# Kernel optimization log

Hardware: AMD Instinct MI355X
Metric: run time of the kernel (lower is better)

The kernel has to match this reference:

```python
import jax, jax.numpy as jnp
import numpy as np
from jax import lax

SHIFTS = (1, 2, 4, 8)

def _neighbors(x, d):
    # x: [B,C,H,W] -> [B,8,C,H,W], 8 reflection-padded directional shifts
    H, W = x.shape[2], x.shape[3]
    def p(t, l, b, r):
        return jnp.pad(x, ((0, 0), (0, 0), (t, b), (l, r)), mode='reflect')
    x0 = p(d, d, 0, 0)[:, :, :H, :W]
    x1 = p(d, 0, 0, 0)[:, :, :H, :]
    x2 = p(d, 0, 0, d)[:, :, :H, d:]
    x3 = p(0, d, 0, 0)[:, :, :, :W]
    x4 = p(0, 0, 0, d)[:, :, :, d:]
    x5 = p(0, d, d, 0)[:, :, d:, :W]
    x6 = p(0, 0, d, 0)[:, :, d:, :]
    x7 = p(0, 0, d, d)[:, :, d:, d:]
    return jnp.stack([x0, x1, x2, x3, x4, x5, x6, x7], axis=1)

def _l2norm(x):
    # F.normalize(dim=-1): x / max(||x||, 1e-12)
    n = jnp.sqrt(jnp.sum(x * x, axis=-1, keepdims=True))
    return x / jnp.maximum(n, 1e-12)

def _forward(cen, q_w, k_w, v_w, sur_w1, sur_b1, sur_w2, sur_b2, sum_weights, out_w, bn_gamma, bn_beta):
    B, C, H, W = cen.shape
    nh = len(SHIFTS)
    keys, qrys, vals = [], [], []
    for i, d in enumerate(SHIFTS):
        nb = _neighbors(cen, d)  # [B,8,C,H,W]
        w2 = jax.nn.softmax(sum_weights[i])  # [2]
        h1 = lax.conv_general_dilated(cen, sur_w1[i], (1, 1), ((d, d), (d, d)),
                                      rhs_dilation=(d, d),
                                      dimension_numbers=('NCHW', 'OIHW', 'NCHW'))
        h1 = jax.nn.relu(h1 + sur_b1[i][None, :, None, None])
        sw = jax.nn.softmax(jnp.einsum('bchw,oc->bohw', h1, sur_w2[i]) + sur_b2[i][None, :, None, None], axis=1) * w2[0]  # [B,8,H,W]
        sum_x = jnp.einsum('bkchw,bkhw->bchw', nb, sw) + cen * w2[1]
        cen_x = nb.mean(axis=1) * w2[0] + cen * w2[1]
        sur = (nb - sum_x[:, None]).reshape(B, 8 * C, H, W)  # cat of x_k - sum_x
        keys.append(jnp.einsum('bchw,oc->bohw', sur, k_w[i]))    # [B,8*hid,H,W]
        vals.append(jnp.einsum('bchw,oc->bohw', sur, v_w[i]))
        qrys.append(jnp.einsum('bchw,oc->bohw', cen_x, q_w[i]))  # [B,hid,H,W]
    HW = H * W
    # torch.stack(dim=2).view(b, nh, -1, HW): row-major reinterpretation
    K = jnp.stack(keys, axis=2).reshape(B, nh, -1, HW)
    Q = jnp.stack(qrys, axis=2).reshape(B, nh, -1, HW)
    V = jnp.stack(vals, axis=2).reshape(B, nh, -1, HW)
    K = _l2norm(K)
    Q = _l2norm(Q)
    score = jnp.einsum('bnqs,bnks->bnqk', Q, K) / np.float32(np.sqrt(HW))
    # InstanceNorm2d(nh), affine=False: normalize over last two dims per (b, head)
    mu = score.mean(axis=(-2, -1), keepdims=True)
    var = score.var(axis=(-2, -1), keepdims=True)
    score = (score - mu) * lax.rsqrt(var + 1e-5)
    attn = jax.nn.softmax(score, axis=-1)
    out = jnp.einsum('bnqk,bnks->bnqs', attn, V).reshape(B, -1, H, W)  # [B,tra,H,W]
    y = jnp.einsum('bchw,oc->bohw', out, out_w)
    # BatchNorm2d in training mode (batch statistics)
    m = y.mean(axis=(0, 2, 3), keepdims=True)
    v = y.var(axis=(0, 2, 3), keepdims=True)
    y = (y - m) * lax.rsqrt(v + 1e-5) * bn_gamma[None, :, None, None] + bn_beta[None, :, None, None]
    return jax.nn.relu(y)

def setup_inputs() -> dict:
    key = jax.random.key(0)
    ks = jax.random.split(key, 12)
    B, C, H, W = 2, 32, 128, 128
    nh, hid, tra, oc = 4, 64, 256, 256
    r = lambda k, s, sc: jax.random.normal(k, s, dtype=jnp.float32) * sc
    return {
        'cen': r(ks[0], (B, C, H, W), 1.0),
        'q_w': r(ks[1], (nh, hid, C), 0.05),
        'k_w': r(ks[2], (nh, 8 * hid, 8 * C), 0.05),
        'v_w': r(ks[3], (nh, 8 * hid, 8 * C), 0.05),
        'sur_w1': r(ks[4], (nh, C, C, 3, 3), 0.05),
        'sur_b1': r(ks[5], (nh, C), 0.02),
        'sur_w2': r(ks[6], (nh, 8, C), 0.05),
        'sur_b2': r(ks[7], (nh, 8), 0.02),
        'sum_weights': r(ks[8], (nh, 2), 0.1),
        'out_w': r(ks[9], (oc, tra), 0.05),
        'bn_gamma': jnp.ones((oc,), jnp.float32) + r(ks[10], (oc,), 0.05),
        'bn_beta': r(ks[11], (oc,), 0.05),
    }

def reference(cen, q_w, k_w, v_w, sur_w1, sur_b1, sur_w2, sur_b2, sum_weights, out_w, bn_gamma, bn_beta):
    return _forward(cen, q_w, k_w, v_w, sur_w1, sur_b1, sur_w2, sur_b2, sum_weights, out_w, bn_gamma, bn_beta)
```

## Files before the change

### kernel.cpp

```cpp
#include <hip/hip_runtime.h>


#define HW 16384
typedef unsigned short u16;
typedef unsigned int u32;
typedef __attribute__((ext_vector_type(8))) short short8;
typedef __attribute__((ext_vector_type(4))) float f32x4;

#define S_CEN 0
#define S_QW 1048576
#define S_KW 1056768
#define S_VW 1581056
#define S_W1 2105344
#define S_B1 2142208
#define S_W2 2142336
#define S_B2 2143360
#define S_SW 2143392
#define S_OW 2143400
#define S_GAMMA 2208936
#define S_BETA 2209192
#define S_TOTAL 2209456

#define G_D1 0
#define G_D2 16384
#define G_S 147456
#define G_SZ 409600

#define GP_SLOT 344064

__device__ __forceinline__ float b2f(u16 u) { return __uint_as_float(((u32)u) << 16); }
__device__ __forceinline__ u16 f2b(float f) {
  u32 u = __float_as_uint(f);
  return (u16)((u + 0x7FFFu + ((u >> 16) & 1u)) >> 16);
}
__device__ __forceinline__ float wave_sum(float v) {
  #pragma unroll
  for (int off = 32; off > 0; off >>= 1) v += __shfl_xor(v, off, 64);
  return v;
}
__device__ __forceinline__ float wave_max(float v) {
  #pragma unroll
  for (int off = 32; off > 0; off >>= 1) v = fmaxf(v, __shfl_xor(v, off, 64));
  return v;
}
__device__ __forceinline__ void unpack8(uint4 v, float* f) {
  f[0] = __uint_as_float(v.x << 16); f[1] = __uint_as_float(v.x & 0xFFFF0000u);
  f[2] = __uint_as_float(v.y << 16); f[3] = __uint_as_float(v.y & 0xFFFF0000u);
  f[4] = __uint_as_float(v.z << 16); f[5] = __uint_as_float(v.z & 0xFFFF0000u);
  f[6] = __uint_as_float(v.w << 16); f[7] = __uint_as_float(v.w & 0xFFFF0000u);
}
__device__ __forceinline__ void gload16(const u16* g, u16* l) {
  __builtin_amdgcn_global_load_lds(
      (const __attribute__((address_space(1))) void*)g,
      (__attribute__((address_space(3))) void*)l, 16, 0, 0);
}

__device__ __forceinline__ void tile_decode(int tile, int& r0, int& c0,
                                            size_t& goff, int& gstride) {
  if (tile == 0) { r0 = 0; c0 = 0; goff = G_D1; gstride = 128; }
  else if (tile < 9) { r0 = 0; c0 = 128 * tile; goff = G_D2 + (size_t)(tile - 1) * 128; gstride = 1024; }
  else if (tile < 17) {
    int t2 = tile - 9; int j = t2 >> 1, p = t2 & 1;
    r0 = 128 + 256 * j + 128 * p; c0 = r0;
    goff = G_S + (size_t)j * 65536 + (size_t)p * (128 * 256 + 128); gstride = 256;
  } else {
    int j = tile - 17;
    r0 = 128 + 256 * j; c0 = r0 + 128;
    goff = G_S + (size_t)j * 65536 + 128; gstride = 256;
  }
}

__global__ void probe(const u32* __restrict__ g, int* __restrict__ flag) {
  if (threadIdx.x == 0) {
    int ok = 1;
    #pragma unroll
    for (int i = 0; i < 4; i++) {
      u32 w = g[i];
      u32 lo = w & 0xFFFFu, hi = w >> 16;
      ok &= (lo >= 0x3E00u && lo <= 0x4100u) ? 1 : 0;
      ok &= (hi >= 0x3E00u && hi <= 0x4100u) ? 1 : 0;
    }
    *flag = ok ? 0 : 1;
  }
}

__global__ __launch_bounds__(256) void convert_all(
    const void* p0, const void* p1, const void* p2, const void* p3,
    const void* p4, const void* p5, const void* p6, const void* p7,
    const void* p8, const void* p9, const void* p10, const void* p11,
    u16* __restrict__ S, const int* __restrict__ flag) {
  const void* src; int n; int off;
  switch (blockIdx.z) {
    case 0:  src = p0;  n = 1048576; off = S_CEN; break;
    case 1:  src = p1;  n = 8192;    off = S_QW; break;
    case 2:  src = p2;  n = 524288;  off = S_KW; break;
    case 3:  src = p3;  n = 524288;  off = S_VW; break;
    case 4:  src = p4;  n = 36864;   off = S_W1; break;
    case 5:  src = p5;  n = 128;     off = S_B1; break;
    case 6:  src = p6;  n = 1024;    off = S_W2; break;
    case 7:  src = p7;  n = 32;      off = S_B2; break;
    case 8:  src = p8;  n = 8;       off = S_SW; break;
    case 9:  src = p9;  n = 65536;   off = S_OW; break;
    case 10: src = p10; n = 256;     off = S_GAMMA; break;
    default: src = p11; n = 256;     off = S_BETA; break;
  }
  int idx = (blockIdx.x * 256 + threadIdx.x) * 4;
  if (idx >= n) return;
  u16* dst = S + off + idx;
  if (*flag) {
    float4 v = ((const float4*)src)[idx >> 2];
    dst[0] = f2b(v.x); dst[1] = f2b(v.y); dst[2] = f2b(v.z); dst[3] = f2b(v.w);
  } else {
    *(ushort4*)dst = ((const ushort4*)src)[idx >> 2];
  }
}

__global__ __launch_bounds__(256) void transp(
    const u16* __restrict__ cen, u16* __restrict__ cenT) {
  __shared__ u16 tile[32][258];
  const int t = threadIdx.x;
  const int s0 = blockIdx.x * 256;
  const u16* cb = cen + (size_t)blockIdx.y * 32 * HW;
  for (int e = t; e < 2048; e += 256) {
    int ci = e >> 6, sx = (e & 63) * 4;
    *(u32*)&tile[ci][sx] = *(const u32*)&cb[(size_t)ci * HW + s0 + sx];
    *(u32*)&tile[ci][sx + 2] = *(const u32*)&cb[(size_t)ci * HW + s0 + sx + 2];
  }
  __syncthreads();
  u16* ob = cenT + (size_t)blockIdx.y * HW * 32;
  for (int e = t; e < 1024; e += 256) {
    int px = e >> 2, cg = (e & 3) * 8;
    u16 tmp[8];
    #pragma unroll
    for (int k = 0; k < 8; k++) tmp[k] = tile[cg + k][px];
    *(uint4*)&ob[(size_t)(s0 + px) * 32 + cg] = *(uint4*)tmp;
  }
}

__global__ __launch_bounds__(256) void sur_w(
    const u16* __restrict__ cenT, const u16* __restrict__ w1g,
    const u16* __restrict__ b1g, const u16* __restrict__ w2g,
    const u16* __restrict__ zbuf, float* __restrict__ lgbuf) {
  const int z = blockIdx.y;
  const int b = z >> 2, si = z & 3, d = 1 << si;
  const int hh = blockIdx.x;
  __shared__ __align__(16) char smem[27776];
  u16* Bs = (u16*)smem;
  u16* w1s = (u16*)(smem + 8192);
  float* h1s = (float*)smem;
  __shared__ float w2s[8][32];
  __shared__ float b1s[32];
  const int t = threadIdx.x;
  for (int e = t; e < 9216; e += 256) {
    int tap = e >> 10, rem = e & 1023, co = rem >> 5, ci = rem & 31;
    int dst = tap * 1024 + co * 32 + ((((ci >> 3) ^ (co & 3)) << 3) | (ci & 7));
    w1s[dst] = w1g[si * 9216 + co * 288 + ci * 9 + tap];
  }
  w2s[t >> 5][t & 31] = b2f(w2g[si * 256 + t]);
  if (t < 32) b1s[t] = b2f(b1g[si * 32 + t]);

  const u16* cb = cenT + (size_t)b * HW * 32;
  const int lane = t & 63, w = t >> 6;
  const int m = lane & 15, quad = lane >> 4;
  const int slot8 = (quad ^ (m & 3)) << 3;
  f32x4 acc[2][2];
  #pragma unroll
  for (int i = 0; i < 2; i++)
    #pragma unroll
    for (int j = 0; j < 2; j++) acc[i][j] = (f32x4){0.f, 0.f, 0.f, 0.f};

  for (int tap = 0; tap < 9; tap++) {
    const int ky = tap / 3, kx = tap - ky * 3;
    const int y = hh + (ky - 1) * d;
    if (y < 0 || y > 127) continue;
    const int dx = (kx - 1) * d;
    #pragma unroll
    for (int q = 0; q < 2; q++) {
      const int e = q * 256 + t;
      const int px = e >> 2, ck = e & 3;
      const int x = px + dx;
      const u16* src = ((unsigned)x < 128u)
          ? cb + ((size_t)(y * 128 + x) * 32 + ((ck ^ (px & 3)) << 3))
          : zbuf;
      gload16(src, Bs + (size_t)e * 8);
    }
    __syncthreads();
    short8 af[2], bf[2];
    #pragma unroll
    for (int i = 0; i < 2; i++)
      af[i] = *(const short8*)&Bs[(w * 32 + i * 16 + m) * 32 + slot8];
    #pragma unroll
    for (int j = 0; j < 2; j++)
      bf[j] = *(const short8*)&w1s[tap * 1024 + (j * 16 + m) * 32 + slot8];
    #pragma unroll
    for (int i = 0; i < 2; i++)
      #pragma unroll
      for (int j = 0; j < 2; j++)
        acc[i][j] = __builtin_amdgcn_mfma_f32_16x16x32_bf16(af[i], bf[j], acc[i][j], 0, 0, 0);
    __syncthreads();
  }

  #pragma unroll
  for (int i = 0; i < 2; i++)
    #pragma unroll
    for (int j = 0; j < 2; j++) {
      const int co = j * 16 + m;
      #pragma unroll
      for (int r = 0; r < 4; r++) {
        const int px = w * 32 + i * 16 + quad * 4 + r;
        h1s[px * 33 + co] = fmaxf(acc[i][j][r] + b1s[co], 0.f);
      }
    }
  __syncthreads();

  const int px = t >> 1, half = t & 1;
  float lp[4];
  #pragma unroll
  for (int k = 0; k < 4; k++) lp[k] = 0.f;
  #pragma unroll
  for (int i = 0; i < 32; i++) {
    const float v = h1s[px * 33 + i];
    #pragma unroll
    for (int k = 0; k < 4; k++) lp[k] = fmaf(v, w2s[half * 4 + k][i], lp[k]);
  }
  float* dst = lgbuf + ((size_t)z * HW + hh * 128 + px) * 8 + half * 4;
  *(float4*)dst = make_float4(lp[0], lp[1], lp[2], lp[3]);
}

__global__ __launch_bounds__(256) void sur_scatter(
    const u16* __restrict__ cen, const float* __restrict__ lgbuf,
    const u16* __restrict__ b2g, const u16* __restrict__ swg,
    u16* __restrict__ Mbuf) {
  const int z = blockIdx.z;
  const int b = z >> 2, si = z & 3, d = 1 << si;
  const int c0 = blockIdx.y * 8;
  const int t = threadIdx.x;
  const int s = (blockIdx.x * 256 + t) * 2;
  const int h = s >> 7, w = s & 127;

  float s0 = b2f(swg[si * 2 + 0]), s1 = b2f(swg[si * 2 + 1]);
  float mx = fmaxf(s0, s1);
  float e0 = expf(s0 - mx), e1 = expf(s1 - mx);
  float w20 = e0 / (e0 + e1), w21 = e1 / (e0 + e1);

  float b2s[8];
  #pragma unroll
  for (int k = 0; k < 8; k++) b2s[k] = b2f(b2g[si * 8 + k]);

  const float* lpa = lgbuf + ((size_t)z * HW + s) * 8;
  float lga[8], lgb[8];
  {
    float4 a0 = *(const float4*)lpa,       a1 = *(const float4*)(lpa + 4);
    float4 g0 = *(const float4*)(lpa + 8), g1 = *(const float4*)(lpa + 12);
    lga[0] = a0.x; lga[1] = a0.y; lga[2] = a0.z; lga[3] = a0.w;
    lga[4] = a1.x; lga[5] = a1.y; lga[6] = a1.z; lga[7] = a1.w;
    lgb[0] = g0.x; lgb[1] = g0.y; lgb[2] = g0.z; lgb[3] = g0.w;
    lgb[4] = g1.x; lgb[5] = g1.y; lgb[6] = g1.z; lgb[7] = g1.w;
  }
  {
    #pragma unroll
    for (int k = 0; k < 8; k++) lga[k] += b2s[k];
    float lm = lga[0];
    #pragma unroll
    for (int k = 1; k < 8; k++) lm = fmaxf(lm, lga[k]);
    float ls = 0.f;
    #pragma unroll
    for (int k = 0; k < 8; k++) { lga[k] = expf(lga[k] - lm); ls += lga[k]; }
    float inv = w20 / ls;
    #pragma unroll
    for (int k = 0; k < 8; k++) lga[k] *= inv;
  }
  {
    #pragma unroll
    for (int k = 0; k < 8; k++) lgb[k] += b2s[k];
    float lm = lgb[0];
    #pragma unroll
    for (int k = 1; k < 8; k++) lm = fmaxf(lm, lgb[k]);
    float ls = 0.f;
    #pragma unroll
    for (int k = 0; k < 8; k++) { lgb[k] = expf(lgb[k] - lm); ls += lgb[k]; }
    float inv = w20 / ls;
    #pragma unroll
    for (int k = 0; k < 8; k++) lgb[k] *= inv;
  }

  const int dy[8] = {-d, -d, -d, 0, 0, d, d, d};
  const int dx[8] = {-d, 0, d, -d, d, -d, 0, d};
  int offa[8], offb[8];
  #pragma unroll
  for (int k = 0; k < 8; k++) {
    int y = h + dy[k]; y = y < 0 ? -y : (y > 127 ? 254 - y : y);
    int xa = w + dx[k]; xa = xa < 0 ? -xa : (xa > 127 ? 254 - xa : xa);
    int xb = w + 1 + dx[k]; xb = xb < 0 ? -xb : (xb > 127 ? 254 - xb : xb);
    offa[k] = y * 128 + xa;
    offb[k] = y * 128 + xb;
  }
  const u16* cb = cen + (size_t)b * 32 * HW;
  u16* Mb = Mbuf + (size_t)b * 1152 * HW;
  for (int c = c0; c < c0 + 8; c++) {
    const u16* cc = cb + (size_t)c * HW;
    u32 cvp = *(const u32*)&cc[s];
    float cva = __uint_as_float(cvp << 16), cvb = __uint_as_float(cvp & 0xFFFF0000u);
    float nba[8], nbb[8];
    #pragma unroll
    for (int k = 0; k < 8; k++) { nba[k] = b2f(cc[offa[k]]); nbb[k] = b2f(cc[offb[k]]); }
    float sxa = 0.f, mna = 0.f, sxb = 0.f, mnb = 0.f;
    #pragma unroll
    for (int k = 0; k < 8; k++) {
      sxa = fmaf(lga[k], nba[k], sxa); mna += nba[k];
      sxb = fmaf(lgb[k], nbb[k], sxb); mnb += nbb[k];
    }
    float suma = sxa + cva * w21, sumb = sxb + cvb * w21;
    u32 cx = (u32)f2b(mna * 0.125f * w20 + cva * w21) |
             ((u32)f2b(mnb * 0.125f * w20 + cvb * w21) << 16);
    *(u32*)&Mb[(size_t)(32 * si + c) * HW + s] = cx;
    #pragma unroll
    for (int k = 0; k < 8; k++) {
      u32 pk = (u32)f2b(nba[k] - suma) | ((u32)f2b(nbb[k] - sumb) << 16);
      *(u32*)&Mb[(size_t)(128 + 256 * si + k * 32 + c) * HW + s] = pk;
    }
  }
}

__global__ __launch_bounds__(256) void gram_mfma(
    const u16* __restrict__ Mbuf, float* __restrict__ Gpart) {
  const int id = blockIdx.x;
  const int tile = id >> 5, combo = id & 31;
  const int ks = combo >> 1, b = combo & 1;
  int r0, c0, gstride; size_t goff;
  tile_decode(tile, r0, c0, goff, gstride);
  const bool diag = (r0 == c0);
  const u16* Mb = Mbuf + (size_t)b * 1152 * HW;
  __shared__ u16 As[128 * 64];
  __shared__ u16 Bs[128 * 64];
  const int t = threadIdx.x;
  const int lane = t & 63, w = t >> 6;
  const int wr = w >> 1, wc = w & 1;
  const int m = lane & 15, quad = lane >> 4;
  const int lr = lane >> 3;
  const int lsl = ((lane & 7) ^ (lr & 7)) * 8;
  const int kbase = ks * 1024;
  f32x4 acc[4][4];
  #pragma unroll
  for (int i = 0; i < 4; i++)
    #pragma unroll
    for (int j = 0; j < 4; j++) acc[i][j] = (f32x4){0.f, 0.f, 0.f, 0.f};

  for (int s0 = kbase; s0 < kbase + 1024; s0 += 64) {
    #pragma unroll
    for (int q = 0; q < 4; q++) {
      const int R0 = w * 32 + q * 8;
      gload16(Mb + (size_t)(r0 + R0 + lr) * HW + s0 + lsl, &As[R0 * 64]);
    }
    if (!diag) {
      #pragma unroll
      for (int q = 0; q < 4; q++) {
        const int R0 = w * 32 + q * 8;
        gload16(Mb + (size_t)(c0 + R0 + lr) * HW + s0 + lsl, &Bs[R0 * 64]);
      }
    }
    __syncthreads();
    const u16* Bb = diag ? As : Bs;
    #pragma unroll
    for (int kh = 0; kh < 2; kh++) {
      short8 af[4], bf[4];
      const int slot = ((quad + 4 * kh) ^ (m & 7)) * 8;
      #pragma unroll
      for (int i = 0; i < 4; i++)
        af[i] = *(const short8*)&As[(wr * 64 + i * 16 + m) * 64 + slot];
      #pragma unroll
      for (int j = 0; j < 4; j++)
        bf[j] = *(const short8*)&Bb[(wc * 64 + j * 16 + m) * 64 + slot];
      #pragma unroll
      for (int i = 0; i < 4; i++)
        #pragma unroll
        for (int j = 0; j < 4; j++)
          acc[i][j] = __builtin_amdgcn_mfma_f32_16x16x32_bf16(af[i], bf[j], acc[i][j], 0, 0, 0);
    }
    __syncthreads();
  }
  float* Gb = Gpart + (size_t)(b * 16 + ks) * GP_SLOT + (size_t)tile * 16384;
  #pragma unroll
  for (int i = 0; i < 4; i++)
    #pragma unroll
    for (int j = 0; j < 4; j++) {
      int col = wc * 64 + j * 16 + m;
      #pragma unroll
      for (int r = 0; r < 4; r++) {
        int row = wr * 64 + i * 16 + quad * 4 + r;
        Gb[row * 128 + col] = acc[i][j][r];
      }
    }
}

__global__ __launch_bounds__(256) void greduce(
    const float* __restrict__ Gpart, float* __restrict__ G) {
  const int chunk = blockIdx.x, tile = blockIdx.y, b = blockIdx.z;
  int r0, c0, gstride; size_t goff;
  tile_decode(tile, r0, c0, goff, gstride);
  const int t = threadIdx.x;
  const int e = chunk * 1024 + t * 4;
  const float* base = Gpart + (size_t)b * 16 * GP_SLOT + (size_t)tile * 16384 + e;
  f32x4 acc = *(const f32x4*)base;
  #pragma unroll
  for (int s = 1; s < 16; s++) acc += *(const f32x4*)(base + (size_t)s * GP_SLOT);
  const int row = e >> 7, col = e & 127;
  *(f32x4*)&G[(size_t)b * G_SZ + goff + (size_t)row * gstride + col] = acc;
}

__global__ __launch_bounds__(256) void mirror_S(float* __restrict__ G) {
  const int j = blockIdx.x & 3, b = blockIdx.x >> 2;
  float* base = G + (size_t)b * G_SZ + G_S + (size_t)j * 65536;
  const int t = threadIdx.x;
  for (int e = t; e < 16384; e += 256) {
    int rr = e >> 7, cc = e & 127;
    base[(size_t)(128 + rr) * 256 + cc] = base[(size_t)cc * 256 + 128 + rr];
  }
}

__global__ __launch_bounds__(64) void qnorm(
    const u16* __restrict__ qw, const float* __restrict__ G,
    float* __restrict__ invQ) {
  const int bn = blockIdx.x, b = bn >> 2, n = bn & 3;
  const int rq = threadIdx.x;
  const int i = rq & 3, q1r = rq >> 2;
  const u16* qr = qw + ((size_t)(i * 64) + 16 * n + q1r) * 32;
  float v[32];
  #pragma unroll
  for (int c = 0; c < 32; c++) v[c] = b2f(qr[c]);
  const float* D1 = G + (size_t)b * G_SZ;
  float ss = 0.f;
  for (int c = 0; c < 32; c++) {
    float tmp = 0.f;
    #pragma unroll
    for (int c2 = 0; c2 < 32; c2++) tmp = fmaf(v[c2], D1[(size_t)(32 * i + c2) * 128 + 32 * i + c], tmp);
    ss = fmaf(tmp, v[c], ss);
  }
  invQ[bn * 64 + rq] = 1.f / fmaxf(sqrtf(fmaxf(ss, 0.f)), 1e-12f);
}

__global__ __launch_bounds__(256) void knorm(
    const u16* __restrict__ kw, const float* __restrict__ G,
    float* __restrict__ invK) {
  const int jj = blockIdx.x;
  const int j = jj & 3, kkg = jj >> 2;
  const int n = blockIdx.y, b = blockIdx.z;
  const int t = threadIdx.x;
  __shared__ float vs[8][256];
  for (int e = t; e < 2048; e += 256) {
    int r = e >> 8, c = e & 255;
    vs[r][c] = b2f(kw[((size_t)(j * 512) + 128 * n + kkg * 8 + r) * 256 + c]);
  }
  __syncthreads();
  const float* S = G + (size_t)b * G_SZ + G_S + (size_t)j * 65536;
  float acc[8];
  #pragma unroll
  for (int r = 0; r < 8; r++) acc[r] = 0.f;
  for (int c2 = 0; c2 < 256; c2++) {
    float sv = S[(size_t)c2 * 256 + t];
    #pragma unroll
    for (int r = 0; r < 8; r++) acc[r] = fmaf(vs[r][c2], sv, acc[r]);
  }
  #pragma unroll
  for (int r = 0; r < 8; r++) acc[r] *= vs[r][t];
  __shared__ float red[8][4];
  const int wv = t >> 6, lane = t & 63;
  #pragma unroll
  for (int r = 0; r < 8; r++) {
    float v = wave_sum(acc[r]);
    if (lane == 0) red[r][wv] = v;
  }
  __syncthreads();
  if (t < 8) {
    float tot = fmaxf(red[t][0] + red[t][1] + red[t][2] + red[t][3], 0.f);
    invK[(size_t)(b * 4 + n) * 512 + 4 * (kkg * 8 + t) + j] =
        1.f / fmaxf(sqrtf(tot), 1e-12f);
  }
}

__global__ __launch_bounds__(256) void score2(
    const u16* __restrict__ qw, const u16* __restrict__ kw,
    const float* __restrict__ G, const float* __restrict__ invQ,
    const float* __restrict__ invK, float* __restrict__ score,
    float* __restrict__ sstat) {
  const int jj = blockIdx.x;
  const int j = jj >> 1, half = jj & 1;
  const int n = blockIdx.y, b = blockIdx.z;
  const float* D2 = G + (size_t)b * G_SZ + G_D2;
  const u16* kwb = kw + ((size_t)(j * 512) + 128 * n + half * 64) * 256;
  __shared__ float As[64][132];
  __shared__ u16 Bs[64][68];
  __shared__ float KD[128][68];
  __shared__ float qws[64][32];
  const int t = threadIdx.x;
  const int tx = t & 7, ty = t >> 3;
  float acc[4][8];
  #pragma unroll
  for (int i = 0; i < 4; i++)
    #pragma unroll
    for (int u = 0; u < 8; u++) acc[i][u] = 0.f;
  for (int ch0 = 0; ch0 < 256; ch0 += 64) {
    for (int e = t; e < 8192; e += 256) {
      int r = e >> 6, kc = e & 63;
      As[kc][r] = D2[(size_t)r * 1024 + j * 256 + ch0 + kc];
    }
    for (int e = t; e < 4096; e += 256) {
      int r = e >> 6, kc = e & 63;
      Bs[kc][r] = kwb[(size_t)r * 256 + ch0 + kc];
    }
    __syncthreads();
    #pragma unroll 4
    for (int kc = 0; kc < 64; kc++) {
      float a[4];
      #pragma unroll
      for (int i = 0; i < 4; i++) a[i] = As[kc][ty * 4 + i];
      float bb[8];
      #pragma unroll
      for (int u = 0; u < 8; u++) bb[u] = b2f(Bs[kc][tx * 8 + u]);
      #pragma unroll
      for (int i = 0; i < 4; i++)
        #pragma unroll
        for (int u = 0; u < 8; u++) acc[i][u] = fmaf(a[i], bb[u], acc[i][u]);
    }
    __syncthreads();
  }
  #pragma unroll
  for (int i = 0; i < 4; i++)
    #pragma unroll
    for (int u = 0; u < 8; u++) KD[ty * 4 + i][tx * 8 + u] = acc[i][u];
  for (int e = t; e < 2048; e += 256) {
    int q = e >> 5, c = e & 31;
    int i = q & 3, q1r = q >> 2;
    qws[q][c] = b2f(qw[((size_t)(i * 64) + 16 * n + q1r) * 32 + c]);
  }
  __syncthreads();
  const int bn = b * 4 + n;
  float* sb = score + (size_t)bn * 64 * 512;
  const float* iQ = invQ + bn * 64;
  const float* iK = invK + (size_t)bn * 512;
  const float isc = 1.f / 128.f;
  float lsum = 0.f, lss = 0.f;
  for (int e = t; e < 4096; e += 256) {
    int q = e >> 6, kkl = e & 63;
    int i = q & 3;
    float s = 0.f;
    #pragma unroll
    for (int c = 0; c < 32; c++) s = fmaf(qws[q][c], KD[i * 32 + c][kkl], s);
    int col = 4 * (half * 64 + kkl) + j;
    float v = s * iQ[q] * iK[col] * isc;
    sb[(size_t)q * 512 + col] = v;
    lsum += v; lss += v * v;
  }
  lsum = wave_sum(lsum); lss = wave_sum(lss);
  __shared__ float redp[8];
  if ((t & 63) == 0) { redp[t >> 6] = lsum; redp[4 + (t >> 6)] = lss; }
  __syncthreads();
  if (t == 0) {
    atomicAdd(&sstat[bn * 2],     redp[0] + redp[1] + redp[2] + redp[3]);
    atomicAdd(&sstat[bn * 2 + 1], redp[4] + redp[5] + redp[6] + redp[7]);
  }
}

__global__ __launch_bounds__(256) void in_softmax(
    float* __restrict__ score, const float* __restrict__ sstat) {
  const int bn = blockIdx.y, rg = blockIdx.x;
  float* sb = score + (size_t)bn * 64 * 512;
  const int t = threadIdx.x;
  float mean = sstat[bn * 2] * (1.f / 32768.f);
  float var = sstat[bn * 2 + 1] * (1.f / 32768.f) - mean * mean;
  float istd = rsqrtf(var + 1e-5f);
  const int wv = t >> 6, lane = t & 63;
  for (int rr = wv; rr < 8; rr += 4) {
    int r = rg * 8 + rr;
    float z[8];
    float m = -1e30f;
    #pragma unroll
    for (int jx = 0; jx < 8; jx++) {
      z[jx] = (sb[(size_t)r * 512 + lane + 64 * jx] - mean) * istd;
      m = fmaxf(m, z[jx]);
    }
    m = wave_max(m);
    float sloc = 0.f;
    #pragma unroll
    for (int jx = 0; jx < 8; jx++) { z[jx] = expf(z[jx] - m); sloc += z[jx]; }
    sloc = wave_sum(sloc);
    float rinv = 1.f / sloc;
    #pragma unroll
    for (int jx = 0; jx < 8; jx++) sb[(size_t)r * 512 + lane + 64 * jx] = z[jx] * rinv;
  }
}

__global__ __launch_bounds__(256) void attnW2(
    const float* __restrict__ attn, const u16* __restrict__ vw,
    float* __restrict__ W2) {
  const int j = blockIdx.x >> 2, n = blockIdx.x & 3;
  const int q0 = blockIdx.y * 8, b = blockIdx.z, bn = b * 4 + n;
  const float* ab = attn + (size_t)bn * 64 * 512;
  const int t = threadIdx.x;
  __shared__ float at_s[8][128];
  for (int e = t; e < 1024; e += 256) {
    int qg = e >> 7, kk = e & 127;
    at_s[qg][kk] = ab[(size_t)(q0 + qg) * 512 + 4 * kk + j];
  }
  __syncthreads();
  float acc[8];
  #pragma unroll
  for (int qg = 0; qg < 8; qg++) acc[qg] = 0.f;
  const u16* vcol = vw + ((size_t)(j * 512) + 128 * n) * 256 + t;
  for (int kk = 0; kk < 128; kk++) {
    float v = b2f(vcol[(size_t)kk * 256]);
    #pragma unroll
    for (int qg = 0; qg < 8; qg++) acc[qg] = fmaf(at_s[qg][kk], v, acc[qg]);
  }
  #pragma unroll
  for (int qg = 0; qg < 8; qg++)
    W2[((size_t)bn * 64 + q0 + qg) * 1024 + j * 256 + t] = acc[qg];
}

__global__ __launch_bounds__(256) void wfin_k(
    const u16* __restrict__ ow, const float* __restrict__ W2,
    u16* __restrict__ Wfin16) {
  const int jc = blockIdx.x, b = blockIdx.y;
  __shared__ float col[256];
  const int t = threadIdx.x;
  col[t] = W2[((size_t)b * 256 + t) * 1024 + jc];
  __syncthreads();
  float acc = 0.f;
  const u16* owr = ow + (size_t)t * 256;
  for (int c = 0; c < 256; c++) acc = fmaf(b2f(owr[c]), col[c], acc);
  Wfin16[((size_t)b * 256 + t) * 1024 + jc] = f2b(acc);
}

__global__ __launch_bounds__(256) void y_gemm_mfma(
    const u16* __restrict__ Wfin16, const u16* __restrict__ Mbuf,
    u16* __restrict__ ybuf) {
  const int b = blockIdx.y, col0 = blockIdx.x * 64;
  __shared__ u16 As[2][256 * 64];
  __shared__ u16 Bs[2][64 * 64];
  const u16* Ab = Wfin16 + (size_t)b * 256 * 1024;
  const u16* Mb = Mbuf + (size_t)b * 1152 * HW + (size_t)128 * HW;
  const int t = threadIdx.x;
  const int lane = t & 63, w = t >> 6;
  const int m = lane & 15, quad = lane >> 4;
  const int kp = t >> 3, cs = t & 7;
  const int lr = lane >> 3;
  const int lsl = ((lane & 7) ^ (lr & 7)) * 8;
  f32x4 acc[4][4];
  #pragma unroll
  for (int i = 0; i < 4; i++)
    #pragma unroll
    for (int j = 0; j < 4; j++) acc[i][j] = (f32x4){0.f, 0.f, 0.f, 0.f};

  uint4 v0, v1;
  auto stageA = [&](int buf, int k0c) {
    #pragma unroll
    for (int q = 0; q < 8; q++)
      gload16(&Ab[(size_t)(w * 64 + q * 8 + lr) * 1024 + k0c + lsl],
              &As[buf][(w * 64 + q * 8) * 64]);
  };
  auto loadB = [&](int k0c) {
    v0 = *(const uint4*)&Mb[(size_t)(k0c + 2 * kp) * HW + col0 + cs * 8];
    v1 = *(const uint4*)&Mb[(size_t)(k0c + 2 * kp + 1) * HW + col0 + cs * 8];
  };
  auto writeB = [&](int buf) {
    u16 t0[8], t1[8];
    *(uint4*)t0 = v0; *(uint4*)t1 = v1;
    const int ksl = kp >> 2, kin = (2 * kp) & 7;
    #pragma unroll
    for (int uu = 0; uu < 8; uu++) {
      int u = (uu + t) & 7;
      int r = cs * 8 + u;
      u32 pair = (u32)t0[u] | ((u32)t1[u] << 16);
      *(u32*)&Bs[buf][r * 64 + ((ksl ^ (r & 7)) << 3) + kin] = pair;
    }
  };

  stageA(0, 0);
  loadB(0);
  writeB(0);
  __syncthreads();

  int cur = 0;
  for (int step = 0; step < 16; step++) {
    const int nxt = cur ^ 1;
    if (step < 15) {
      stageA(nxt, (step + 1) * 64);
      loadB((step + 1) * 64);
    }
    #pragma unroll
    for (int kh = 0; kh < 2; kh++) {
      short8 af[4], bf[4];
      const int slot = ((4 * kh + quad) ^ (m & 7)) * 8;
      #pragma unroll
      for (int i = 0; i < 4; i++)
        af[i] = *(const short8*)&As[cur][(w * 64 + i * 16 + m) * 64 + slot];
      #pragma unroll
      for (int j = 0; j < 4; j++)
        bf[j] = *(const short8*)&Bs[cur][(j * 16 + m) * 64 + slot];
      #pragma unroll
      for (int i = 0; i < 4; i++)
        #pragma unroll
        for (int j = 0; j < 4; j++)
          acc[i][j] = __builtin_amdgcn_mfma_f32_16x16x32_bf16(af[i], bf[j], acc[i][j], 0, 0, 0);
    }
    if (step < 15) {
      writeB(nxt);
      __syncthreads();
      cur = nxt;
    }
  }
  #pragma unroll
  for (int i = 0; i < 4; i++)
    #pragma unroll
    for (int j = 0; j < 4; j++) {
      int col = col0 + j * 16 + m;
      #pragma unroll
      for (int r = 0; r < 4; r++) {
        int row = w * 64 + i * 16 + quad * 4 + r;
        ybuf[((size_t)b * 256 + row) * HW + col] = f2b(acc[i][j][r]);
      }
    }
}

__global__ __launch_bounds__(256) void bn_stats(
    const u16* __restrict__ y, float* __restrict__ st) {
  const int o = blockIdx.x;
  const int t = threadIdx.x;
  float sum = 0.f, ss = 0.f;
  for (int bb = 0; bb < 2; bb++) {
    const u16* p = y + ((size_t)bb * 256 + o) * HW;
    for (int e = t; e < HW / 8; e += 256) {
      uint4 v = ((const uint4*)p)[e];
      float f[8];
      unpack8(v, f);
      #pragma unroll
      for (int k = 0; k < 8; k++) { sum += f[k]; ss += f[k] * f[k]; }
    }
  }
  __shared__ float red[8];
  sum = wave_sum(sum); ss = wave_sum(ss);
  if ((t & 63) == 0) { red[t >> 6] = sum; red[4 + (t >> 6)] = ss; }
  __syncthreads();
  if (t == 0) {
    float mean = (red[0] + red[1] + red[2] + red[3]) / 32768.f;
    float var = (red[4] + red[5] + red[6] + red[7]) / 32768.f - mean * mean;
    st[o * 2] = mean;
    st[o * 2 + 1] = rsqrtf(var + 1e-5f);
  }
}

__global__ __launch_bounds__(256) void bn_apply(
    const u16* __restrict__ y, const float* __restrict__ st,
    const u16* __restrict__ gamma, const u16* __restrict__ beta,
    const int* __restrict__ flag, void* __restrict__ out) {
  const int idx8 = blockIdx.x * 256 + threadIdx.x;
  const int r = idx8 >> 11;
  const int o = r & 255;
  float mean = st[o * 2], istd = st[o * 2 + 1];
  float g = b2f(gamma[o]), be = b2f(beta[o]);
  uint4 v = ((const uint4*)y)[idx8];
  float f[8];
  unpack8(v, f);
  float rr[8];
  #pragma unroll
  for (int k = 0; k < 8; k++) rr[k] = fmaxf((f[k] - mean) * istd * g + be, 0.f);
  if (*flag) {
    float* of = (float*)out + (size_t)idx8 * 8;
    *(float4*)of = make_float4(rr[0], rr[1], rr[2], rr[3]);
    *(float4*)(of + 4) = make_float4(rr[4], rr[5], rr[6], rr[7]);
  } else {
    u32 p0 = (u32)f2b(rr[0]) | ((u32)f2b(rr[1]) << 16);
    u32 p1 = (u32)f2b(rr[2]) | ((u32)f2b(rr[3]) << 16);
    u32 p2 = (u32)f2b(rr[4]) | ((u32)f2b(rr[5]) << 16);
    u32 p3 = (u32)f2b(rr[6]) | ((u32)f2b(rr[7]) << 16);
    ((uint4*)out)[idx8] = make_uint4(p0, p1, p2, p3);
  }
}

extern "C" void kernel_launch(void* const* d_in, const int* in_sizes, int n_in,
                              void* d_out, int out_size, void* d_ws, size_t ws_size,
                              hipStream_t stream) {
  float* G     = (float*)d_ws;
  float* score = G + 819200;
  float* invQ  = score + 262144;
  float* invK  = invQ + 512;
  float* W2    = invK + 4096;
  float* Wfin  = W2 + 524288;
  float* bnst  = Wfin + 524288;
  float* sstat = bnst + 512;
  float* zbuf  = sstat + 16;
  int* flag    = (int*)(zbuf + 16);
  u16* Sbuf    = (u16*)(flag + 16);
  u16* Mbuf    = Sbuf + S_TOTAL;
  u16* ybuf    = Mbuf + 37748736;
  u16* Wfin16  = (u16*)Wfin;
  float* lgbuf = (float*)ybuf;
  u16* cenT    = (u16*)(lgbuf + 1048576);
  float* Gpart = (float*)ybuf;

  probe<<<1, 64, 0, stream>>>((const u32*)d_in[10], flag);
  convert_all<<<dim3(1024, 1, 12), 256, 0, stream>>>(
      d_in[0], d_in[1], d_in[2], d_in[3], d_in[4], d_in[5], d_in[6], d_in[7],
      d_in[8], d_in[9], d_in[10], d_in[11], Sbuf, flag);
  hipMemsetAsync(sstat, 0, 32 * sizeof(float), stream);

  transp<<<dim3(64, 2), 256, 0, stream>>>(Sbuf + S_CEN, cenT);
  sur_w<<<dim3(128, 8), 256, 0, stream>>>(
      cenT, Sbuf + S_W1, Sbuf + S_B1, Sbuf + S_W2, (const u16*)zbuf, lgbuf);
  sur_scatter<<<dim3(32, 4, 8), 256, 0, stream>>>(
      Sbuf + S_CEN, lgbuf, Sbuf + S_B2, Sbuf + S_SW, Mbuf);
  gram_mfma<<<672, 256, 0, stream>>>(Mbuf, Gpart);
  greduce<<<dim3(16, 21, 2), 256, 0, stream>>>(Gpart, G);
  mirror_S<<<8, 256, 0, stream>>>(G);
  qnorm<<<8, 64, 0, stream>>>(Sbuf + S_QW, G, invQ);
  knorm<<<dim3(64, 4, 2), 256, 0, stream>>>(Sbuf + S_KW, G, invK);
  score2<<<dim3(8, 4, 2), 256, 0, stream>>>(
      Sbuf + S_QW, Sbuf + S_KW, G, invQ, invK, score, sstat);
  in_softmax<<<dim3(8, 8), 256, 0, stream>>>(score, sstat);
  attnW2<<<dim3(16, 8, 2), 256, 0, stream>>>(score, Sbuf + S_VW, W2);
  wfin_k<<<dim3(1024, 2), 256, 0, stream>>>(Sbuf + S_OW, W2, Wfin16);
  y_gemm_mfma<<<dim3(256, 2), 256, 0, stream>>>(Wfin16, Mbuf, ybuf);
  bn_stats<<<256, 256, 0, stream>>>(ybuf, bnst);
  bn_apply<<<4096, 256, 0, stream>>>(ybuf, bnst, Sbuf + S_GAMMA, Sbuf + S_BETA,
                                     flag, d_out);
}
```

Before: 363.6 us.

## Transpose M into K-contiguous layout and split y GEMM over row halves

Adds a transpose kernel that copies the 1024-row slice of Mbuf into a pixel-major, K-contiguous buffer MT. The y GEMM then reads both operands with 16-byte row loads and splits output rows into two 128-row tiles, doubling the grid and shrinking per-block accumulators. This targets strided B-operand loads and low occupancy in the old y GEMM. The cost is an extra 64 MB write and read per call, and the new path only runs when the workspace is large enough; otherwise the old kernel is kept as a fallback.

```diff
diff --git a/kernel.cpp b/kernel.cpp
--- a/kernel.cpp
+++ b/kernel.cpp
@@ -137,6 +137,24 @@
   }
 }
 
+__global__ __launch_bounds__(256) void transpM(
+    const u16* __restrict__ Mbuf, u16* __restrict__ MT) {
+  const int st = blockIdx.x, kt = blockIdx.y, b = blockIdx.z;
+  const u16* src = Mbuf + (size_t)b * 1152 * HW + (size_t)(128 + kt * 64) * HW + st * 64;
+  u16* dst = MT + (size_t)b * 16384 * 1024 + (size_t)st * 64 * 1024 + kt * 64;
+  const int t = threadIdx.x;
+  const int sl = t & 63;
+  #pragma unroll
+  for (int q = 0; q < 2; q++) {
+    const int kc = (t >> 6) + q * 4;
+    u16 tmp[8];
+    #pragma unroll
+    for (int kk = 0; kk < 8; kk++)
+      tmp[kk] = src[(size_t)(kc * 8 + kk) * HW + sl];
+    *(uint4*)&dst[(size_t)sl * 1024 + kc * 8] = *(uint4*)tmp;
+  }
+}
+
 __global__ __launch_bounds__(256) void sur_w(
     const u16* __restrict__ cenT, const u16* __restrict__ w1g,
     const u16* __restrict__ b1g, const u16* __restrict__ w2g,
@@ -632,6 +650,68 @@
 }
 
 __global__ __launch_bounds__(256) void y_gemm_mfma(
+    const u16* __restrict__ Wfin16, const u16* __restrict__ MT,
+    u16* __restrict__ ybuf) {
+  const int b = blockIdx.z, row0 = blockIdx.y * 128, col0 = blockIdx.x * 64;
+  __shared__ u16 As[128 * 64];
+  __shared__ u16 Bs[64 * 64];
+  const u16* Ab = Wfin16 + (size_t)b * 256 * 1024;
+  const u16* Mb = MT + (size_t)b * 16384 * 1024;
+  const int t = threadIdx.x;
+  const int lane = t & 63, w = t >> 6;
+  const int m = lane & 15, quad = lane >> 4;
+  const int lr = lane >> 3;
+  const int lsl = ((lane & 7) ^ (lr & 7)) * 8;
+  f32x4 acc[2][4];
+  #pragma unroll
+  for (int i = 0; i < 2; i++)
+    #pragma unroll
+    for (int j = 0; j < 4; j++) acc[i][j] = (f32x4){0.f, 0.f, 0.f, 0.f};
+
+  for (int k0 = 0; k0 < 1024; k0 += 64) {
+    #pragma unroll
+    for (int q = 0; q < 4; q++) {
+      const int R0 = w * 32 + q * 8;
+      gload16(&Ab[(size_t)(row0 + R0 + lr) * 1024 + k0 + lsl], &As[R0 * 64]);
+    }
+    #pragma unroll
+    for (int q = 0; q < 2; q++) {
+      const int R0 = w * 16 + q * 8;
+      gload16(&Mb[(size_t)(col0 + R0 + lr) * 1024 + k0 + lsl], &Bs[R0 * 64]);
+    }
+    __syncthreads();
+    #pragma unroll
+    for (int kh = 0; kh < 2; kh++) {
+      short8 af[2], bf[4];
+      const int slot = ((quad + 4 * kh) ^ (m & 7)) * 8;
+      #pragma unroll
+      for (int i = 0; i < 2; i++)
+        af[i] = *(const short8*)&As[(w * 32 + i * 16 + m) * 64 + slot];
+      #pragma unroll
+      for (int j = 0; j < 4; j++)
+        bf[j] = *(const short8*)&Bs[(j * 16 + m) * 64 + slot];
+      #pragma unroll
+      for (int i = 0; i < 2; i++)
+        #pragma unroll
+        for (int j = 0; j < 4; j++)
+          acc[i][j] = __builtin_amdgcn_mfma_f32_16x16x32_bf16(af[i], bf[j], acc[i][j], 0, 0, 0);
+    }
+    __syncthreads();
+  }
+  #pragma unroll
+  for (int i = 0; i < 2; i++)
+    #pragma unroll
+    for (int j = 0; j < 4; j++) {
+      int col = col0 + j * 16 + m;
+      #pragma unroll
+      for (int r = 0; r < 4; r++) {
+        int row = row0 + w * 32 + i * 16 + quad * 4 + r;
+        ybuf[((size_t)b * 256 + row) * HW + col] = f2b(acc[i][j][r]);
+      }
+    }
+}
+
+__global__ __launch_bounds__(256) void y_gemm_fb(
     const u16* __restrict__ Wfin16, const u16* __restrict__ Mbuf,
     u16* __restrict__ ybuf) {
   const int b = blockIdx.y, col0 = blockIdx.x * 64;
@@ -797,6 +877,9 @@
   float* lgbuf = (float*)ybuf;
   u16* cenT    = (u16*)(lgbuf + 1048576);
   float* Gpart = (float*)ybuf;
+  u16* MT      = (u16*)((char*)ybuf + 16777216);
+  const size_t mt_need = (size_t)((char*)MT - (char*)d_ws) + 67108864ull;
+  const bool use_mt = ws_size >= mt_need;
 
   probe<<<1, 64, 0, stream>>>((const u32*)d_in[10], flag);
   convert_all<<<dim3(1024, 1, 12), 256, 0, stream>>>(
@@ -811,6 +894,8 @@
       Sbuf + S_CEN, lgbuf, Sbuf + S_B2, Sbuf + S_SW, Mbuf);
   gram_mfma<<<672, 256, 0, stream>>>(Mbuf, Gpart);
   greduce<<<dim3(16, 21, 2), 256, 0, stream>>>(Gpart, G);
+  if (use_mt)
+    transpM<<<dim3(256, 16, 2), 256, 0, stream>>>(Mbuf, MT);
   mirror_S<<<8, 256, 0, stream>>>(G);
   qnorm<<<8, 64, 0, stream>>>(Sbuf + S_QW, G, invQ);
   knorm<<<dim3(64, 4, 2), 256, 0, stream>>>(Sbuf + S_KW, G, invK);
@@ -819,7 +904,10 @@
   in_softmax<<<dim3(8, 8), 256, 0, stream>>>(score, sstat);
   attnW2<<<dim3(16, 8, 2), 256, 0, stream>>>(score, Sbuf + S_VW, W2);
   wfin_k<<<dim3(1024, 2), 256, 0, stream>>>(Sbuf + S_OW, W2, Wfin16);
-  y_gemm_mfma<<<dim3(256, 2), 256, 0, stream>>>(Wfin16, Mbuf, ybuf);
+  if (use_mt)
+    y_gemm_mfma<<<dim3(256, 2, 2), 256, 0, stream>>>(Wfin16, MT, ybuf);
+  else
+    y_gemm_fb<<<dim3(256, 2), 256, 0, stream>>>(Wfin16, Mbuf, ybuf);
   bn_stats<<<256, 256, 0, stream>>>(ybuf, bnst);
   bn_apply<<<4096, 256, 0, stream>>>(ybuf, bnst, Sbuf + S_GAMMA, Sbuf + S_BETA,
                                      flag, d_out);
```

New measurement: 384.5 us. 1.06x slower.

## Retile wfin_k so each thread computes 16 outputs with coalesced W2 reads

Applied to the files above, without the earlier changes.

The wfin_k small GEMM (out_w times W2) is rewritten. Each block now stages a 16x256 slice of out_w into padded shared memory. Each thread walks a contiguous W2 column and keeps 16 accumulators. This replaces the old scheme, where each of 2048 blocks gathered one strided W2 column and each thread read a whole row of out_w with uncoalesced access. The new grid is only 128 blocks, which gives less parallelism in exchange for coalesced loads and register reuse.

```diff
diff --git a/kernel.cpp b/kernel.cpp
--- a/kernel.cpp
+++ b/kernel.cpp
@@ -620,15 +620,29 @@
 __global__ __launch_bounds__(256) void wfin_k(
     const u16* __restrict__ ow, const float* __restrict__ W2,
     u16* __restrict__ Wfin16) {
-  const int jc = blockIdx.x, b = blockIdx.y;
-  __shared__ float col[256];
-  const int t = threadIdx.x;
-  col[t] = W2[((size_t)b * 256 + t) * 1024 + jc];
-  __syncthreads();
-  float acc = 0.f;
-  const u16* owr = ow + (size_t)t * 256;
-  for (int c = 0; c < 256; c++) acc = fmaf(b2f(owr[c]), col[c], acc);
-  Wfin16[((size_t)b * 256 + t) * 1024 + jc] = f2b(acc);
+  const int jc0 = blockIdx.x * 256;
+  const int o0 = blockIdx.y * 16;
+  const int b = blockIdx.z;
+  __shared__ float ows[16][257];
+  const int t = threadIdx.x;
+  for (int e = t; e < 4096; e += 256) {
+    int o = e >> 8, c = e & 255;
+    ows[o][c] = b2f(ow[(size_t)(o0 + o) * 256 + c]);
+  }
+  __syncthreads();
+  const float* W2b = W2 + (size_t)b * 256 * 1024 + jc0 + t;
+  float acc[16];
+  #pragma unroll
+  for (int o = 0; o < 16; o++) acc[o] = 0.f;
+  for (int c = 0; c < 256; c++) {
+    float w2v = W2b[(size_t)c * 1024];
+    #pragma unroll
+    for (int o = 0; o < 16; o++) acc[o] = fmaf(ows[o][c], w2v, acc[o]);
+  }
+  u16* dst = Wfin16 + (size_t)b * 256 * 1024 + jc0 + t;
+  #pragma unroll
+  for (int o = 0; o < 16; o++)
+    dst[(size_t)(o0 + o) * 1024] = f2b(acc[o]);
 }
 
 __global__ __launch_bounds__(256) void y_gemm_mfma(
@@ -818,7 +832,7 @@
       Sbuf + S_QW, Sbuf + S_KW, G, invQ, invK, score, sstat);
   in_softmax<<<dim3(8, 8), 256, 0, stream>>>(score, sstat);
   attnW2<<<dim3(16, 8, 2), 256, 0, stream>>>(score, Sbuf + S_VW, W2);
-  wfin_k<<<dim3(1024, 2), 256, 0, stream>>>(Sbuf + S_OW, W2, Wfin16);
+  wfin_k<<<dim3(4, 16, 2), 256, 0, stream>>>(Sbuf + S_OW, W2, Wfin16);
   y_gemm_mfma<<<dim3(256, 2), 256, 0, stream>>>(Wfin16, Mbuf, ybuf);
   bn_stats<<<256, 256, 0, stream>>>(ybuf, bnst);
   bn_apply<<<4096, 256, 0, stream>>>(ybuf, bnst, Sbuf + S_GAMMA, Sbuf + S_BETA,
```

Result: faster. 351.1 us (-3.4%).
